# Kernel optimization log

Hardware: AMD Instinct MI355X
Metric: run time of the kernel (lower is better)

Reference implementation:

```python
import jax, jax.numpy as jnp
import numpy as np
import math

N_HEADS, INPUT_DIM, EMBED_DIM = 8, 512, 512
KEY_DIM = EMBED_DIM // N_HEADS  # val_dim == key_dim == 64
B, NQ, G = 4, 2048, 2048


def setup_inputs() -> dict:
    key = jax.random.key(0)
    ks = jax.random.split(key, 7)
    stdv_k = 1.0 / math.sqrt(KEY_DIM)
    stdv_e = 1.0 / math.sqrt(EMBED_DIM)
    return {
        "q": jax.random.normal(ks[0], (B, NQ, INPUT_DIM), jnp.float32),
        "h": jax.random.normal(ks[1], (B, G, INPUT_DIM), jnp.float32),
        "mask": jax.random.randint(ks[2], (B, NQ, G), 0, 2) == 1,  # True = attention not possible
        "W_query": jax.random.uniform(ks[3], (N_HEADS, INPUT_DIM, KEY_DIM), jnp.float32, -stdv_k, stdv_k),
        "W_key": jax.random.uniform(ks[4], (N_HEADS, INPUT_DIM, KEY_DIM), jnp.float32, -stdv_k, stdv_k),
        "W_val": jax.random.uniform(ks[5], (N_HEADS, INPUT_DIM, KEY_DIM), jnp.float32, -stdv_k, stdv_k),
        "W_out": jax.random.uniform(ks[6], (N_HEADS, KEY_DIM, EMBED_DIM), jnp.float32, -stdv_e, stdv_e),
    }


def reference(q, h, mask, W_query, W_key, W_val, W_out):
    norm = 1.0 / math.sqrt(KEY_DIM)
    # Per-head projections: (H, B, S, kd)
    Q = jnp.einsum("bqd,hdk->hbqk", q, W_query)
    K = jnp.einsum("bgd,hdk->hbgk", h, W_key)
    V = jnp.einsum("bgd,hdv->hbgv", h, W_val)
    # Full attention scores: (H, B, NQ, G)
    comp = norm * jnp.einsum("hbqk,hbgk->hbqg", Q, K)
    m = mask[None]  # (1, B, NQ, G) broadcasts over heads
    comp = jnp.where(m, -jnp.inf, comp)
    attn = jax.nn.softmax(comp, axis=-1)
    attn = jnp.where(m, 0.0, attn)  # mirrors the clone + zero step (also fixes all-masked rows)
    heads = jnp.einsum("hbqg,hbgv->hbqv", attn, V)
    # Output projection: flatten heads and apply W_out (H, vd, E)
    out = jnp.einsum("hbqv,hve->bqe", heads, W_out)
    return out
```

## Files before the change

### kernel.cpp

```cpp
#include <hip/hip_runtime.h>
#include <hip/hip_bf16.h>
#include <stdint.h>

#define NHEADS 8
#define INDIM 512
#define EMB 512
#define BSZ 4
#define NQS 2048
#define GS 2048

#define ALPHA_F 0.18033688011112042f

#if __has_builtin(__builtin_amdgcn_exp2f)
#define EXP2(x) __builtin_amdgcn_exp2f(x)
#else
#define EXP2(x) __expf((x)*0.69314718056f)
#endif

typedef short bf16x8 __attribute__((ext_vector_type(8)));
typedef float f32x4 __attribute__((ext_vector_type(4)));

static __device__ __forceinline__ unsigned short f2bf(float f) {
  unsigned int u = __builtin_bit_cast(unsigned int, f);
  unsigned int rounding = 0x7FFFu + ((u >> 16) & 1u);
  u += rounding;
  return (unsigned short)(u >> 16);
}

typedef __attribute__((address_space(3))) void lds_void;
typedef __attribute__((address_space(1))) const void gm_void;
static __device__ __forceinline__ void gll16(const void* g, void* s) {
  __builtin_amdgcn_global_load_lds((gm_void*)g, (lds_void*)s, 16, 0, 0);
}

__global__ void k_prep(const float4* __restrict__ q, const float4* __restrict__ h,
                       const void* __restrict__ mask,
                       const float* __restrict__ wq, const float* __restrict__ wk,
                       const float* __restrict__ wv, const float* __restrict__ wo,
                       ushort4* __restrict__ qb, ushort4* __restrict__ hb,
                       unsigned short* __restrict__ wqt, unsigned short* __restrict__ wkvt,
                       unsigned short* __restrict__ wot, unsigned short* __restrict__ maskB16) {
  int blk = blockIdx.x, t = threadIdx.x;
  if (blk < 2048) {
    const float4* src = blk < 1024 ? q : h;
    ushort4* dst = blk < 1024 ? qb : hb;
    int base = (blk & 1023) * 256 + t;
#pragma unroll
    for (int i = 0; i < 4; i++) {
      int idx = base + i * 262144;
      float4 v = src[idx];
      ushort4 o;
      o.x = f2bf(v.x); o.y = f2bf(v.y); o.z = f2bf(v.z); o.w = f2bf(v.w);
      dst[idx] = o;
    }
  } else if (blk < 3072) {
    const unsigned int* m32h = (const unsigned int*)mask;
    bool bytes = __ballot(m32h[t & 63] > 1u) != 0ull;
    int base = (blk - 2048) * 256 + t;
#pragma unroll
    for (int i = 0; i < 4; i++) {
      int widx = base + i * 262144;
      unsigned int bits = 0;
      if (bytes) {
        const uchar4* p = (const uchar4*)((const unsigned char*)mask + (size_t)widx * 16);
#pragma unroll
        for (int j = 0; j < 4; j++) {
          uchar4 v = p[j];
          bits |= ((v.x ? 1u : 0u) << (4 * j)) | ((v.y ? 1u : 0u) << (4 * j + 1)) |
                  ((v.z ? 1u : 0u) << (4 * j + 2)) | ((v.w ? 1u : 0u) << (4 * j + 3));
        }
      } else {
        const int4* p = (const int4*)((const int*)mask + (size_t)widx * 16);
#pragma unroll
        for (int j = 0; j < 4; j++) {
          int4 v = p[j];
          bits |= ((v.x ? 1u : 0u) << (4 * j)) | ((v.y ? 1u : 0u) << (4 * j + 1)) |
                  ((v.z ? 1u : 0u) << (4 * j + 2)) | ((v.w ? 1u : 0u) << (4 * j + 3));
        }
      }
      maskB16[widx] = (unsigned short)bits;
    }
  } else {
    int id = (blk - 3072) * 256 + t;
#pragma unroll
    for (int i = 0; i < 8; i++) {
      int e = id * 8 + i;
      int which = e >> 18, r = e & 262143;
      int k = r & 511, n = r >> 9;
      int hh = n >> 6, j = n & 63;
      if (which == 0) wqt[r] = f2bf(wq[hh * 32768 + k * 64 + j] * ALPHA_F);
      else if (which == 1) wkvt[r] = f2bf(wk[hh * 32768 + k * 64 + j]);
      else if (which == 2) wkvt[262144 + r] = f2bf(wv[hh * 32768 + k * 64 + j]);
      else wot[r] = f2bf(wo[k * 512 + n]);
    }
  }
}


template <int MODE>
__global__ __launch_bounds__(256) void k_gemm3(const unsigned short* __restrict__ A,
                                               const unsigned short* __restrict__ Bt,
                                               void* __restrict__ C, void* __restrict__ C2) {
  __shared__ unsigned short As[2][4096];
  __shared__ unsigned short Bs[2][8192];
  int m0 = blockIdx.x * 64, n0 = blockIdx.y * 128;
  int t = threadIdx.x;
  int w = t >> 6, l = t & 63, c = l & 15, lg = l >> 4;
  int wr = w >> 1, wc = w & 1;

  int rbA = t >> 7, kcc = (t >> 4) & 7, cc = t & 15;
  const unsigned short* aG = A + (size_t)(m0 + rbA * 16 + cc) * 512 + kcc * 8;
  const unsigned short* bG = Bt + (size_t)(n0 + rbA * 16 + cc) * 512 + kcc * 8;
  int ldsOff = w * 1024 + (t & 63) * 16;

  f32x4 acc[2][4];
#pragma unroll
  for (int mi = 0; mi < 2; mi++)
#pragma unroll
    for (int ni = 0; ni < 4; ni++) acc[mi][ni] = {0.f, 0.f, 0.f, 0.f};

  gll16(aG, (char*)As[0] + ldsOff);
  gll16(aG + 32 * 512, (char*)As[0] + ldsOff + 4096);
  gll16(bG, (char*)Bs[0] + ldsOff);
  gll16(bG + 32 * 512, (char*)Bs[0] + ldsOff + 4096);
  gll16(bG + 64 * 512, (char*)Bs[0] + ldsOff + 8192);
  gll16(bG + 96 * 512, (char*)Bs[0] + ldsOff + 12288);

  for (int kk = 0; kk < 8; kk++) {
    int cur = kk & 1;
    asm volatile("s_waitcnt vmcnt(0)" ::: "memory");
    __builtin_amdgcn_s_barrier();
    if (kk < 7) {
      int ko = (kk + 1) * 64;
      gll16(aG + ko, (char*)As[cur ^ 1] + ldsOff);
      gll16(aG + ko + 32 * 512, (char*)As[cur ^ 1] + ldsOff + 4096);
      gll16(bG + ko, (char*)Bs[cur ^ 1] + ldsOff);
      gll16(bG + ko + 32 * 512, (char*)Bs[cur ^ 1] + ldsOff + 4096);
      gll16(bG + ko + 64 * 512, (char*)Bs[cur ^ 1] + ldsOff + 8192);
      gll16(bG + ko + 96 * 512, (char*)Bs[cur ^ 1] + ldsOff + 12288);
    }
    bf16x8 af[2][2], bfr[4][2];
#pragma unroll
    for (int kc = 0; kc < 2; kc++) {
#pragma unroll
      for (int mi = 0; mi < 2; mi++)
        af[mi][kc] = *(const bf16x8*)((const char*)As[cur] + ((wr * 2 + mi) * 128 + (kc * 4 + lg) * 16 + c) * 16);
#pragma unroll
      for (int ni = 0; ni < 4; ni++)
        bfr[ni][kc] = *(const bf16x8*)((const char*)Bs[cur] + ((wc * 4 + ni) * 128 + (kc * 4 + lg) * 16 + c) * 16);
    }
#pragma unroll
    for (int kc = 0; kc < 2; kc++)
#pragma unroll
      for (int mi = 0; mi < 2; mi++)
#pragma unroll
        for (int ni = 0; ni < 4; ni++)
          acc[mi][ni] = __builtin_amdgcn_mfma_f32_16x16x32_bf16(af[mi][kc], bfr[ni][kc], acc[mi][ni], 0, 0, 0);
  }

#pragma unroll
  for (int mi = 0; mi < 2; mi++)
#pragma unroll
    for (int ni = 0; ni < 4; ni++) {
      int row = m0 + wr * 32 + mi * 16 + 4 * lg;
      int col = n0 + wc * 64 + ni * 16 + c;
#pragma unroll
      for (int r = 0; r < 4; r++)
        ((float*)C)[(size_t)(row + r) * 512 + col] = acc[mi][ni][r];
    }
}

__global__ __launch_bounds__(256) void k_gemmQKV(const unsigned short* __restrict__ qb_,
                                                 const unsigned short* __restrict__ hb_,
                                                 const unsigned short* __restrict__ wqt,
                                                 const unsigned short* __restrict__ wkvt,
                                                 unsigned short* __restrict__ Qp,
                                                 unsigned short* __restrict__ Kp,
                                                 unsigned short* __restrict__ Vt) {
  __shared__ unsigned short As[2][4096];
  __shared__ unsigned short Bs[2][8192];
  int ny = blockIdx.y;
  const unsigned short* A = (ny < 4) ? qb_ : hb_;
  const unsigned short* Bt = (ny < 4) ? wqt : wkvt;
  int n0 = (ny < 4) ? ny * 128 : (ny - 4) * 128;
  int m0 = blockIdx.x * 64;
  int t = threadIdx.x;
  int w = t >> 6, l = t & 63, c = l & 15, lg = l >> 4;
  int wr = w >> 1, wc = w & 1;

  int rbA = t >> 7, kcc = (t >> 4) & 7, cc = t & 15;
  const unsigned short* aG = A + (size_t)(m0 + rbA * 16 + cc) * 512 + kcc * 8;
  const unsigned short* bG = Bt + (size_t)(n0 + rbA * 16 + cc) * 512 + kcc * 8;
  int ldsOff = w * 1024 + (t & 63) * 16;

  f32x4 acc[2][4];
#pragma unroll
  for (int mi = 0; mi < 2; mi++)
#pragma unroll
    for (int ni = 0; ni < 4; ni++) acc[mi][ni] = {0.f, 0.f, 0.f, 0.f};

  gll16(aG, (char*)As[0] + ldsOff);
  gll16(aG + 32 * 512, (char*)As[0] + ldsOff + 4096);
  gll16(bG, (char*)Bs[0] + ldsOff);
  gll16(bG + 32 * 512, (char*)Bs[0] + ldsOff + 4096);
  gll16(bG + 64 * 512, (char*)Bs[0] + ldsOff + 8192);
  gll16(bG + 96 * 512, (char*)Bs[0] + ldsOff + 12288);

  for (int kk = 0; kk < 8; kk++) {
    int cur = kk & 1;
    asm volatile("s_waitcnt vmcnt(0)" ::: "memory");
    __builtin_amdgcn_s_barrier();
    if (kk < 7) {
      int ko = (kk + 1) * 64;
      gll16(aG + ko, (char*)As[cur ^ 1] + ldsOff);
      gll16(aG + ko + 32 * 512, (char*)As[cur ^ 1] + ldsOff + 4096);
      gll16(bG + ko, (char*)Bs[cur ^ 1] + ldsOff);
      gll16(bG + ko + 32 * 512, (char*)Bs[cur ^ 1] + ldsOff + 4096);
      gll16(bG + ko + 64 * 512, (char*)Bs[cur ^ 1] + ldsOff + 8192);
      gll16(bG + ko + 96 * 512, (char*)Bs[cur ^ 1] + ldsOff + 12288);
    }
    bf16x8 af[2][2], bfr[4][2];
#pragma unroll
    for (int kc = 0; kc < 2; kc++) {
#pragma unroll
      for (int mi = 0; mi < 2; mi++)
        af[mi][kc] = *(const bf16x8*)((const char*)As[cur] + ((wr * 2 + mi) * 128 + (kc * 4 + lg) * 16 + c) * 16);
#pragma unroll
      for (int ni = 0; ni < 4; ni++)
        bfr[ni][kc] = *(const bf16x8*)((const char*)Bs[cur] + ((wc * 4 + ni) * 128 + (kc * 4 + lg) * 16 + c) * 16);
    }
#pragma unroll
    for (int kc = 0; kc < 2; kc++)
#pragma unroll
      for (int mi = 0; mi < 2; mi++)
#pragma unroll
        for (int ni = 0; ni < 4; ni++)
          acc[mi][ni] = __builtin_amdgcn_mfma_f32_16x16x32_bf16(af[mi][kc], bfr[ni][kc], acc[mi][ni], 0, 0, 0);
  }

#pragma unroll
  for (int mi = 0; mi < 2; mi++)
#pragma unroll
    for (int ni = 0; ni < 4; ni++) {
      int row = m0 + wr * 32 + mi * 16 + 4 * lg;
      int col = n0 + wc * 64 + ni * 16 + c;
      if (ny < 4) {
#pragma unroll
        for (int r = 0; r < 4; r++)
          Qp[(size_t)(row + r) * 512 + col] = f2bf(acc[mi][ni][r]);
      } else if (col < 512) {
#pragma unroll
        for (int r = 0; r < 4; r++)
          Kp[(size_t)(row + r) * 512 + col] = f2bf(acc[mi][ni][r]);
      } else {
        int col5 = col - 512, hd2 = col5 >> 6, vv = col5 & 63;
        int bb = row >> 11, g = row & 2047;
        ushort4 u;
        u.x = f2bf(acc[mi][ni][0]);
        u.y = f2bf(acc[mi][ni][1]);
        u.z = f2bf(acc[mi][ni][2]);
        u.w = f2bf(acc[mi][ni][3]);
        *(ushort4*)(Vt + (size_t)((bb * 8 + hd2) * 64 + vv) * GS + g) = u;
      }
    }
}

__global__ __launch_bounds__(256) void k_attn6(const unsigned short* __restrict__ Qp,
                                               const unsigned short* __restrict__ Kp,
                                               const unsigned short* __restrict__ Vt,
                                               const unsigned short* __restrict__ maskB16,
                                               unsigned short* __restrict__ Hd) {
  __shared__ unsigned short Ksh[2][8192];
  __shared__ unsigned short Vsh[2][8192];
  __shared__ unsigned short Plds[4][2048];

  int bid = blockIdx.x;
  int fid = (bid & 7) * 64 + (bid >> 3);
  int qtile = fid & 15;
  int bh = fid >> 4;
  int b = bh >> 3, hd = bh & 7;

  int t = threadIdx.x;
  int w = t >> 6, l = t & 63, c = l & 15, lg = l >> 4;
  int qw = qtile * 128 + w * 32;

  bf16x8 qb[2][2];
#pragma unroll
  for (int qt = 0; qt < 2; qt++)
#pragma unroll
    for (int kc = 0; kc < 2; kc++)
      qb[qt][kc] = *(const bf16x8*)(Qp + (size_t)(b * NQS + qw + qt * 16 + c) * 512 + hd * 64 + kc * 32 + lg * 8);

  int sr = ((t >> 7) & 1) * 16 + (t & 15);
  int sdc = ((t >> 6) & 1) * 4 + ((t >> 4) & 3);
  const unsigned short* kgbase = Kp + (size_t)(b * GS + sr) * 512 + hd * 64 + sdc * 8;
  const unsigned short* vgbase = Vt + (size_t)(bh * 64 + sr) * GS + sdc * 8;
  char* kdst[2] = {(char*)&Ksh[0][0] + w * 1024, (char*)&Ksh[1][0] + w * 1024};
  char* vdst[2] = {(char*)&Vsh[0][0] + w * 1024, (char*)&Vsh[1][0] + w * 1024};

  f32x4 o[4][2];
#pragma unroll
  for (int vt = 0; vt < 4; vt++) { o[vt][0] = {0.f, 0.f, 0.f, 0.f}; o[vt][1] = {0.f, 0.f, 0.f, 0.f}; }
  float lrow[2] = {0.f, 0.f};

  const ulonglong2* mp0 = (const ulonglong2*)(maskB16 + (size_t)(b * NQS + qw + c) * 128);
  const ulonglong2* mp1 = (const ulonglong2*)(maskB16 + (size_t)(b * NQS + qw + 16 + c) * 128);

#pragma unroll
  for (int hh = 0; hh < 2; hh++) {
    const unsigned short* kg = kgbase + (size_t)(hh * 64) * 512;
    const unsigned short* vg = vgbase + hh * 64;
    gll16(kg, kdst[0] + hh * 8192);
    gll16(kg + 32 * 512, kdst[0] + hh * 8192 + 4096);
    gll16(vg, vdst[0] + hh * 8192);
    gll16(vg + 32 * GS, vdst[0] + hh * 8192 + 4096);
  }
  ulonglong2 m0 = mp0[0], m1 = mp1[0];
  ulonglong2 m0n = m0, m1n = m1;

  for (int kt = 0; kt < 16; kt++) {
    int cur = kt & 1;
    asm volatile("s_waitcnt vmcnt(0)" ::: "memory");
    __builtin_amdgcn_s_barrier();
    if (kt < 15) {
      size_t g0 = (size_t)(kt + 1) * 128;
#pragma unroll
      for (int hh = 0; hh < 2; hh++) {
        const unsigned short* kg = kgbase + (g0 + hh * 64) * 512;
        const unsigned short* vg = vgbase + g0 + hh * 64;
        char* kd = kdst[cur ^ 1] + hh * 8192;
        char* vd = vdst[cur ^ 1] + hh * 8192;
        gll16(kg, kd);
        gll16(kg + 32 * 512, kd + 4096);
        gll16(vg, vd);
        gll16(vg + 32 * GS, vd + 4096);
      }
      m0n = mp0[kt + 1];
      m1n = mp1[kt + 1];
    }

    f32x4 s0[4][2], s1[4][2];
#pragma unroll
    for (int gt = 0; gt < 4; gt++) {
      s0[gt][0] = {0.f, 0.f, 0.f, 0.f}; s0[gt][1] = {0.f, 0.f, 0.f, 0.f};
      s1[gt][0] = {0.f, 0.f, 0.f, 0.f}; s1[gt][1] = {0.f, 0.f, 0.f, 0.f};
    }
    const unsigned short* Kc0 = &Ksh[cur][0];
    const unsigned short* Kc1 = &Ksh[cur][4096];
    __builtin_amdgcn_s_setprio(1);
#pragma unroll
    for (int kc = 0; kc < 2; kc++) {
      bf16x8 ka[4];
#pragma unroll
      for (int gt = 0; gt < 4; gt++)
        ka[gt] = *(const bf16x8*)(Kc0 + ((gt * 2 + kc) * 64 + l) * 8);
#pragma unroll
      for (int gt = 0; gt < 4; gt++) {
        s0[gt][0] = __builtin_amdgcn_mfma_f32_16x16x32_bf16(ka[gt], qb[0][kc], s0[gt][0], 0, 0, 0);
        s0[gt][1] = __builtin_amdgcn_mfma_f32_16x16x32_bf16(ka[gt], qb[1][kc], s0[gt][1], 0, 0, 0);
      }
    }
#pragma unroll
    for (int kc = 0; kc < 2; kc++) {
      bf16x8 ka[4];
#pragma unroll
      for (int gt = 0; gt < 4; gt++)
        ka[gt] = *(const bf16x8*)(Kc1 + ((gt * 2 + kc) * 64 + l) * 8);
#pragma unroll
      for (int gt = 0; gt < 4; gt++) {
        s1[gt][0] = __builtin_amdgcn_mfma_f32_16x16x32_bf16(ka[gt], qb[0][kc], s1[gt][0], 0, 0, 0);
        s1[gt][1] = __builtin_amdgcn_mfma_f32_16x16x32_bf16(ka[gt], qb[1][kc], s1[gt][1], 0, 0, 0);
      }
    }
    __builtin_amdgcn_s_setprio(0);

#pragma unroll
    for (int qt = 0; qt < 2; qt++) {
      unsigned long long wmq = qt ? m1.x : m0.x;
      float ls = 0.f;
#pragma unroll
      for (int gt = 0; gt < 4; gt++) {
        unsigned nib = (unsigned)(wmq >> (gt * 16));
        f32x4 pv;
#pragma unroll
        for (int r = 0; r < 4; r++) {
          float e = EXP2(s0[gt][qt][r]);
          pv[r] = ((nib >> (4 * lg + r)) & 1u) ? 0.f : e;
          ls += pv[r];
        }
        s0[gt][qt] = pv;
      }
      lrow[qt] += ls;
#pragma unroll
      for (int gt = 0; gt < 4; gt++) {
        uint2 wp;
        asm("v_cvt_pk_bf16_f32 %0, %1, %2" : "=v"(wp.x) : "v"(s0[gt][qt][0]), "v"(s0[gt][qt][1]));
        asm("v_cvt_pk_bf16_f32 %0, %1, %2" : "=v"(wp.y) : "v"(s0[gt][qt][2]), "v"(s0[gt][qt][3]));
        int chunk = (qt * 2 + (gt >> 1)) * 64 + ((gt & 1) * 2 + (lg >> 1)) * 16 + c;
        *(uint2*)((char*)&Plds[w][0] + chunk * 16 + 8 * (lg & 1)) = wp;
      }
    }

#pragma unroll
    for (int qt = 0; qt < 2; qt++) {
      unsigned long long wmq = qt ? m1.y : m0.y;
      float ls = 0.f;
#pragma unroll
      for (int gt = 0; gt < 4; gt++) {
        unsigned nib = (unsigned)(wmq >> (gt * 16));
        f32x4 pv;
#pragma unroll
        for (int r = 0; r < 4; r++) {
          float e = EXP2(s1[gt][qt][r]);
          pv[r] = ((nib >> (4 * lg + r)) & 1u) ? 0.f : e;
          ls += pv[r];
        }
        s1[gt][qt] = pv;
      }
      lrow[qt] += ls;
    }

    asm volatile("s_waitcnt lgkmcnt(0)" ::: "memory");
    __builtin_amdgcn_sched_barrier(0);

    {
      const unsigned short* Vc = &Vsh[cur][0];
      __builtin_amdgcn_s_setprio(1);
#pragma unroll
      for (int kc2 = 0; kc2 < 2; kc2++) {
        bf16x8 pb[2];
#pragma unroll
        for (int qt = 0; qt < 2; qt++)
          pb[qt] = *(const bf16x8*)((const char*)&Plds[w][0] + ((qt * 2 + kc2) * 64 + l) * 16);
        bf16x8 va[4];
#pragma unroll
        for (int vt = 0; vt < 4; vt++)
          va[vt] = *(const bf16x8*)(Vc + ((vt * 2 + kc2) * 64 + l) * 8);
#pragma unroll
        for (int vt = 0; vt < 4; vt++) {
          o[vt][0] = __builtin_amdgcn_mfma_f32_16x16x32_bf16(va[vt], pb[0], o[vt][0], 0, 0, 0);
          o[vt][1] = __builtin_amdgcn_mfma_f32_16x16x32_bf16(va[vt], pb[1], o[vt][1], 0, 0, 0);
        }
      }
      __builtin_amdgcn_s_setprio(0);
    }
    __builtin_amdgcn_sched_barrier(0);

#pragma unroll
    for (int qt = 0; qt < 2; qt++)
#pragma unroll
      for (int gt = 0; gt < 4; gt++) {
        uint2 wp;
        asm("v_cvt_pk_bf16_f32 %0, %1, %2" : "=v"(wp.x) : "v"(s1[gt][qt][0]), "v"(s1[gt][qt][1]));
        asm("v_cvt_pk_bf16_f32 %0, %1, %2" : "=v"(wp.y) : "v"(s1[gt][qt][2]), "v"(s1[gt][qt][3]));
        int chunk = (qt * 2 + (gt >> 1)) * 64 + ((gt & 1) * 2 + (lg >> 1)) * 16 + c;
        *(uint2*)((char*)&Plds[w][0] + chunk * 16 + 8 * (lg & 1)) = wp;
      }
    asm volatile("s_waitcnt lgkmcnt(0)" ::: "memory");
    __builtin_amdgcn_sched_barrier(0);

    {
      const unsigned short* Vc = &Vsh[cur][4096];
      __builtin_amdgcn_s_setprio(1);
#pragma unroll
      for (int kc2 = 0; kc2 < 2; kc2++) {
        bf16x8 pb[2];
#pragma unroll
        for (int qt = 0; qt < 2; qt++)
          pb[qt] = *(const bf16x8*)((const char*)&Plds[w][0] + ((qt * 2 + kc2) * 64 + l) * 16);
        bf16x8 va[4];
#pragma unroll
        for (int vt = 0; vt < 4; vt++)
          va[vt] = *(const bf16x8*)(Vc + ((vt * 2 + kc2) * 64 + l) * 8);
#pragma unroll
        for (int vt = 0; vt < 4; vt++) {
          o[vt][0] = __builtin_amdgcn_mfma_f32_16x16x32_bf16(va[vt], pb[0], o[vt][0], 0, 0, 0);
          o[vt][1] = __builtin_amdgcn_mfma_f32_16x16x32_bf16(va[vt], pb[1], o[vt][1], 0, 0, 0);
        }
      }
      __builtin_amdgcn_s_setprio(0);
    }
    m0 = m0n;
    m1 = m1n;
  }

#pragma unroll
  for (int qt = 0; qt < 2; qt++) {
    float lr = lrow[qt];
    lr += __shfl_xor(lr, 16);
    lr += __shfl_xor(lr, 32);
    float inv = lr > 0.f ? 1.0f / lr : 0.f;
    int q = qw + qt * 16 + c;
#pragma unroll
    for (int vt = 0; vt < 4; vt++) {
      ushort4 u;
      u.x = f2bf(o[vt][qt][0] * inv);
      u.y = f2bf(o[vt][qt][1] * inv);
      u.z = f2bf(o[vt][qt][2] * inv);
      u.w = f2bf(o[vt][qt][3] * inv);
      *(ushort4*)(Hd + (size_t)(b * NQS + q) * 512 + hd * 64 + vt * 16 + 4 * lg) = u;
    }
  }
}


extern "C" void kernel_launch(void* const* d_in, const int* in_sizes, int n_in,
                              void* d_out, int out_size, void* d_ws, size_t ws_size,
                              hipStream_t stream) {
  const float* q = (const float*)d_in[0];
  const float* h = (const float*)d_in[1];
  const void* mask = d_in[2];
  const float* wq = (const float*)d_in[3];
  const float* wk = (const float*)d_in[4];
  const float* wv = (const float*)d_in[5];
  const float* wo = (const float*)d_in[6];
  float* out = (float*)d_out;

  unsigned short* qb_ = (unsigned short*)d_ws;
  unsigned short* hb_ = qb_ + 8192 * 512;
  unsigned short* Qp = hb_ + 8192 * 512;
  unsigned short* Kp = Qp + 8192 * 512;
  unsigned short* Vtp = Kp + 8192 * 512;
  unsigned short* Hd = Vtp + 8192 * 512;
  unsigned short* wqt = Hd + 8192 * 512;
  unsigned short* wkvt = wqt + 512 * 512;
  unsigned short* wot = wkvt + 1024 * 512;
  unsigned short* maskB16 = wot + 512 * 512;

  k_prep<<<3584, 256, 0, stream>>>((const float4*)q, (const float4*)h, mask, wq, wk, wv, wo,
                                   (ushort4*)qb_, (ushort4*)hb_, wqt, wkvt, wot, maskB16);
  dim3 gqkv(128, 12);
  k_gemmQKV<<<gqkv, 256, 0, stream>>>(qb_, hb_, wqt, wkvt, Qp, Kp, Vtp);
  k_attn6<<<512, 256, 0, stream>>>(Qp, Kp, Vtp, maskB16, Hd);
  dim3 go(128, 4);
  k_gemm3<1><<<go, 256, 0, stream>>>(Hd, wot, out, nullptr);
}
```

Baseline: 145.3 us.

## Rewrite attention with 32x32 MFMA, register-resident P, direct global K/V loads

Replaces the LDS double-buffered attention kernel with one that uses 32x32x16 MFMA tiles. K and V are read directly from global memory into registers, so there is no shared-memory staging and no block barriers. The probability matrix is repacked in registers with v_permlane32_swap instead of a round-trip through LDS. This removes LDS traffic and synchronization, but relies on cache hits for repeated K/V reads across waves and loses explicit prefetch overlap.

```diff
diff --git a/kernel.cpp b/kernel.cpp
--- a/kernel.cpp
+++ b/kernel.cpp
@@ -19,6 +19,8 @@
 
 typedef short bf16x8 __attribute__((ext_vector_type(8)));
 typedef float f32x4 __attribute__((ext_vector_type(4)));
+typedef float f32x16 __attribute__((ext_vector_type(16)));
+typedef unsigned int u32x4 __attribute__((ext_vector_type(4)));
 
 static __device__ __forceinline__ unsigned short f2bf(float f) {
   unsigned int u = __builtin_bit_cast(unsigned int, f);
@@ -95,7 +97,6 @@
     }
   }
 }
-
 
 template <int MODE>
 __global__ __launch_bounds__(256) void k_gemm3(const unsigned short* __restrict__ A,
@@ -265,15 +266,11 @@
     }
 }
 
-__global__ __launch_bounds__(256) void k_attn6(const unsigned short* __restrict__ Qp,
-                                               const unsigned short* __restrict__ Kp,
-                                               const unsigned short* __restrict__ Vt,
-                                               const unsigned short* __restrict__ maskB16,
-                                               unsigned short* __restrict__ Hd) {
-  __shared__ unsigned short Ksh[2][8192];
-  __shared__ unsigned short Vsh[2][8192];
-  __shared__ unsigned short Plds[4][2048];
-
+__global__ __launch_bounds__(256, 2) void k_attn7(const unsigned short* __restrict__ Qp,
+                                                  const unsigned short* __restrict__ Kp,
+                                                  const unsigned short* __restrict__ Vt,
+                                                  const unsigned short* __restrict__ maskB16,
+                                                  unsigned short* __restrict__ Hd) {
   int bid = blockIdx.x;
   int fid = (bid & 7) * 64 + (bid >> 3);
   int qtile = fid & 15;
@@ -281,224 +278,92 @@
   int b = bh >> 3, hd = bh & 7;
 
   int t = threadIdx.x;
-  int w = t >> 6, l = t & 63, c = l & 15, lg = l >> 4;
-  int qw = qtile * 128 + w * 32;
-
-  bf16x8 qb[2][2];
-#pragma unroll
-  for (int qt = 0; qt < 2; qt++)
-#pragma unroll
-    for (int kc = 0; kc < 2; kc++)
-      qb[qt][kc] = *(const bf16x8*)(Qp + (size_t)(b * NQS + qw + qt * 16 + c) * 512 + hd * 64 + kc * 32 + lg * 8);
-
-  int sr = ((t >> 7) & 1) * 16 + (t & 15);
-  int sdc = ((t >> 6) & 1) * 4 + ((t >> 4) & 3);
-  const unsigned short* kgbase = Kp + (size_t)(b * GS + sr) * 512 + hd * 64 + sdc * 8;
-  const unsigned short* vgbase = Vt + (size_t)(bh * 64 + sr) * GS + sdc * 8;
-  char* kdst[2] = {(char*)&Ksh[0][0] + w * 1024, (char*)&Ksh[1][0] + w * 1024};
-  char* vdst[2] = {(char*)&Vsh[0][0] + w * 1024, (char*)&Vsh[1][0] + w * 1024};
-
-  f32x4 o[4][2];
-#pragma unroll
-  for (int vt = 0; vt < 4; vt++) { o[vt][0] = {0.f, 0.f, 0.f, 0.f}; o[vt][1] = {0.f, 0.f, 0.f, 0.f}; }
-  float lrow[2] = {0.f, 0.f};
-
-  const ulonglong2* mp0 = (const ulonglong2*)(maskB16 + (size_t)(b * NQS + qw + c) * 128);
-  const ulonglong2* mp1 = (const ulonglong2*)(maskB16 + (size_t)(b * NQS + qw + 16 + c) * 128);
-
-#pragma unroll
-  for (int hh = 0; hh < 2; hh++) {
-    const unsigned short* kg = kgbase + (size_t)(hh * 64) * 512;
-    const unsigned short* vg = vgbase + hh * 64;
-    gll16(kg, kdst[0] + hh * 8192);
-    gll16(kg + 32 * 512, kdst[0] + hh * 8192 + 4096);
-    gll16(vg, vdst[0] + hh * 8192);
-    gll16(vg + 32 * GS, vdst[0] + hh * 8192 + 4096);
+  int w = t >> 6, l = t & 63;
+  int lo = l & 31, hi = l >> 5;
+  int hi4 = hi * 4;
+  int q = qtile * 128 + w * 32 + lo;
+
+  const unsigned short* qrow = Qp + (size_t)(b * NQS + q) * 512 + hd * 64 + hi * 8;
+  bf16x8 qf[4];
+#pragma unroll
+  for (int s = 0; s < 4; s++) qf[s] = *(const bf16x8*)(qrow + s * 16);
+
+  const unsigned short* krow = Kp + (size_t)(b * GS + lo) * 512 + hd * 64 + hi * 8;
+  const unsigned short* vrow0 = Vt + (size_t)(bh * 64 + lo) * GS + hi * 8;
+  const unsigned short* vrow1 = Vt + (size_t)(bh * 64 + 32 + lo) * GS + hi * 8;
+  const unsigned long long* mrow = (const unsigned long long*)maskB16 + (size_t)(b * NQS + q) * 32;
+
+  f32x16 o0, o1;
+#pragma unroll
+  for (int i = 0; i < 16; i++) { o0[i] = 0.f; o1[i] = 0.f; }
+  float ls[4] = {0.f, 0.f, 0.f, 0.f};
+
+  for (int kt = 0; kt < 32; kt++) {
+    unsigned long long wm = mrow[kt];
+#pragma unroll
+    for (int g2 = 0; g2 < 2; g2++) {
+      int gbase = kt * 64 + g2 * 32;
+      f32x16 sreg;
+#pragma unroll
+      for (int i = 0; i < 16; i++) sreg[i] = 0.f;
+#pragma unroll
+      for (int s = 0; s < 4; s++) {
+        bf16x8 ka = *(const bf16x8*)(krow + (size_t)gbase * 512 + s * 16);
+        sreg = __builtin_amdgcn_mfma_f32_32x32x16_bf16(ka, qf[s], sreg, 0, 0, 0);
+      }
+      unsigned int mbits = (unsigned int)(wm >> (g2 * 32));
+      float p[16];
+#pragma unroll
+      for (int r = 0; r < 16; r++) {
+        float e = EXP2(sreg[r]);
+        unsigned bit = (mbits >> ((r & 3) + 8 * (r >> 2) + hi4)) & 1u;
+        p[r] = bit ? 0.f : e;
+        ls[r & 3] += p[r];
+      }
+      unsigned int cw0, cw1, cw2, cw3, cw4, cw5, cw6, cw7;
+      asm("v_cvt_pk_bf16_f32 %0, %1, %2" : "=v"(cw0) : "v"(p[0]), "v"(p[1]));
+      asm("v_cvt_pk_bf16_f32 %0, %1, %2" : "=v"(cw1) : "v"(p[2]), "v"(p[3]));
+      asm("v_cvt_pk_bf16_f32 %0, %1, %2" : "=v"(cw2) : "v"(p[4]), "v"(p[5]));
+      asm("v_cvt_pk_bf16_f32 %0, %1, %2" : "=v"(cw3) : "v"(p[6]), "v"(p[7]));
+      asm("v_cvt_pk_bf16_f32 %0, %1, %2" : "=v"(cw4) : "v"(p[8]), "v"(p[9]));
+      asm("v_cvt_pk_bf16_f32 %0, %1, %2" : "=v"(cw5) : "v"(p[10]), "v"(p[11]));
+      asm("v_cvt_pk_bf16_f32 %0, %1, %2" : "=v"(cw6) : "v"(p[12]), "v"(p[13]));
+      asm("v_cvt_pk_bf16_f32 %0, %1, %2" : "=v"(cw7) : "v"(p[14]), "v"(p[15]));
+      asm("v_permlane32_swap_b32 %0, %1" : "+v"(cw0), "+v"(cw2));
+      asm("v_permlane32_swap_b32 %0, %1" : "+v"(cw1), "+v"(cw3));
+      asm("v_permlane32_swap_b32 %0, %1" : "+v"(cw4), "+v"(cw6));
+      asm("v_permlane32_swap_b32 %0, %1" : "+v"(cw5), "+v"(cw7));
+      u32x4 pw0 = {cw0, cw1, cw2, cw3};
+      u32x4 pw1 = {cw4, cw5, cw6, cw7};
+      bf16x8 pb0 = __builtin_bit_cast(bf16x8, pw0);
+      bf16x8 pb1 = __builtin_bit_cast(bf16x8, pw1);
+      bf16x8 va00 = *(const bf16x8*)(vrow0 + gbase);
+      bf16x8 va10 = *(const bf16x8*)(vrow1 + gbase);
+      bf16x8 va01 = *(const bf16x8*)(vrow0 + gbase + 16);
+      bf16x8 va11 = *(const bf16x8*)(vrow1 + gbase + 16);
+      o0 = __builtin_amdgcn_mfma_f32_32x32x16_bf16(va00, pb0, o0, 0, 0, 0);
+      o1 = __builtin_amdgcn_mfma_f32_32x32x16_bf16(va10, pb0, o1, 0, 0, 0);
+      o0 = __builtin_amdgcn_mfma_f32_32x32x16_bf16(va01, pb1, o0, 0, 0, 0);
+      o1 = __builtin_amdgcn_mfma_f32_32x32x16_bf16(va11, pb1, o1, 0, 0, 0);
+    }
   }
-  ulonglong2 m0 = mp0[0], m1 = mp1[0];
-  ulonglong2 m0n = m0, m1n = m1;
-
-  for (int kt = 0; kt < 16; kt++) {
-    int cur = kt & 1;
-    asm volatile("s_waitcnt vmcnt(0)" ::: "memory");
-    __builtin_amdgcn_s_barrier();
-    if (kt < 15) {
-      size_t g0 = (size_t)(kt + 1) * 128;
-#pragma unroll
-      for (int hh = 0; hh < 2; hh++) {
-        const unsigned short* kg = kgbase + (g0 + hh * 64) * 512;
-        const unsigned short* vg = vgbase + g0 + hh * 64;
-        char* kd = kdst[cur ^ 1] + hh * 8192;
-        char* vd = vdst[cur ^ 1] + hh * 8192;
-        gll16(kg, kd);
-        gll16(kg + 32 * 512, kd + 4096);
-        gll16(vg, vd);
-        gll16(vg + 32 * GS, vd + 4096);
-      }
-      m0n = mp0[kt + 1];
-      m1n = mp1[kt + 1];
-    }
-
-    f32x4 s0[4][2], s1[4][2];
-#pragma unroll
-    for (int gt = 0; gt < 4; gt++) {
-      s0[gt][0] = {0.f, 0.f, 0.f, 0.f}; s0[gt][1] = {0.f, 0.f, 0.f, 0.f};
-      s1[gt][0] = {0.f, 0.f, 0.f, 0.f}; s1[gt][1] = {0.f, 0.f, 0.f, 0.f};
-    }
-    const unsigned short* Kc0 = &Ksh[cur][0];
-    const unsigned short* Kc1 = &Ksh[cur][4096];
-    __builtin_amdgcn_s_setprio(1);
-#pragma unroll
-    for (int kc = 0; kc < 2; kc++) {
-      bf16x8 ka[4];
-#pragma unroll
-      for (int gt = 0; gt < 4; gt++)
-        ka[gt] = *(const bf16x8*)(Kc0 + ((gt * 2 + kc) * 64 + l) * 8);
-#pragma unroll
-      for (int gt = 0; gt < 4; gt++) {
-        s0[gt][0] = __builtin_amdgcn_mfma_f32_16x16x32_bf16(ka[gt], qb[0][kc], s0[gt][0], 0, 0, 0);
-        s0[gt][1] = __builtin_amdgcn_mfma_f32_16x16x32_bf16(ka[gt], qb[1][kc], s0[gt][1], 0, 0, 0);
-      }
-    }
-#pragma unroll
-    for (int kc = 0; kc < 2; kc++) {
-      bf16x8 ka[4];
-#pragma unroll
-      for (int gt = 0; gt < 4; gt++)
-        ka[gt] = *(const bf16x8*)(Kc1 + ((gt * 2 + kc) * 64 + l) * 8);
-#pragma unroll
-      for (int gt = 0; gt < 4; gt++) {
-        s1[gt][0] = __builtin_amdgcn_mfma_f32_16x16x32_bf16(ka[gt], qb[0][kc], s1[gt][0], 0, 0, 0);
-        s1[gt][1] = __builtin_amdgcn_mfma_f32_16x16x32_bf16(ka[gt], qb[1][kc], s1[gt][1], 0, 0, 0);
-      }
-    }
-    __builtin_amdgcn_s_setprio(0);
-
-#pragma unroll
-    for (int qt = 0; qt < 2; qt++) {
-      unsigned long long wmq = qt ? m1.x : m0.x;
-      float ls = 0.f;
-#pragma unroll
-      for (int gt = 0; gt < 4; gt++) {
-        unsigned nib = (unsigned)(wmq >> (gt * 16));
-        f32x4 pv;
-#pragma unroll
-        for (int r = 0; r < 4; r++) {
-          float e = EXP2(s0[gt][qt][r]);
-          pv[r] = ((nib >> (4 * lg + r)) & 1u) ? 0.f : e;
-          ls += pv[r];
-        }
-        s0[gt][qt] = pv;
-      }
-      lrow[qt] += ls;
-#pragma unroll
-      for (int gt = 0; gt < 4; gt++) {
-        uint2 wp;
-        asm("v_cvt_pk_bf16_f32 %0, %1, %2" : "=v"(wp.x) : "v"(s0[gt][qt][0]), "v"(s0[gt][qt][1]));
-        asm("v_cvt_pk_bf16_f32 %0, %1, %2" : "=v"(wp.y) : "v"(s0[gt][qt][2]), "v"(s0[gt][qt][3]));
-        int chunk = (qt * 2 + (gt >> 1)) * 64 + ((gt & 1) * 2 + (lg >> 1)) * 16 + c;
-        *(uint2*)((char*)&Plds[w][0] + chunk * 16 + 8 * (lg & 1)) = wp;
-      }
-    }
-
-#pragma unroll
-    for (int qt = 0; qt < 2; qt++) {
-      unsigned long long wmq = qt ? m1.y : m0.y;
-      float ls = 0.f;
-#pragma unroll
-      for (int gt = 0; gt < 4; gt++) {
-        unsigned nib = (unsigned)(wmq >> (gt * 16));
-        f32x4 pv;
-#pragma unroll
-        for (int r = 0; r < 4; r++) {
-          float e = EXP2(s1[gt][qt][r]);
-          pv[r] = ((nib >> (4 * lg + r)) & 1u) ? 0.f : e;
-          ls += pv[r];
-        }
-        s1[gt][qt] = pv;
-      }
-      lrow[qt] += ls;
-    }
-
-    asm volatile("s_waitcnt lgkmcnt(0)" ::: "memory");
-    __builtin_amdgcn_sched_barrier(0);
-
-    {
-      const unsigned short* Vc = &Vsh[cur][0];
-      __builtin_amdgcn_s_setprio(1);
-#pragma unroll
-      for (int kc2 = 0; kc2 < 2; kc2++) {
-        bf16x8 pb[2];
-#pragma unroll
-        for (int qt = 0; qt < 2; qt++)
-          pb[qt] = *(const bf16x8*)((const char*)&Plds[w][0] + ((qt * 2 + kc2) * 64 + l) * 16);
-        bf16x8 va[4];
-#pragma unroll
-        for (int vt = 0; vt < 4; vt++)
-          va[vt] = *(const bf16x8*)(Vc + ((vt * 2 + kc2) * 64 + l) * 8);
-#pragma unroll
-        for (int vt = 0; vt < 4; vt++) {
-          o[vt][0] = __builtin_amdgcn_mfma_f32_16x16x32_bf16(va[vt], pb[0], o[vt][0], 0, 0, 0);
-          o[vt][1] = __builtin_amdgcn_mfma_f32_16x16x32_bf16(va[vt], pb[1], o[vt][1], 0, 0, 0);
-        }
-      }
-      __builtin_amdgcn_s_setprio(0);
-    }
-    __builtin_amdgcn_sched_barrier(0);
-
-#pragma unroll
-    for (int qt = 0; qt < 2; qt++)
-#pragma unroll
-      for (int gt = 0; gt < 4; gt++) {
-        uint2 wp;
-        asm("v_cvt_pk_bf16_f32 %0, %1, %2" : "=v"(wp.x) : "v"(s1[gt][qt][0]), "v"(s1[gt][qt][1]));
-        asm("v_cvt_pk_bf16_f32 %0, %1, %2" : "=v"(wp.y) : "v"(s1[gt][qt][2]), "v"(s1[gt][qt][3]));
-        int chunk = (qt * 2 + (gt >> 1)) * 64 + ((gt & 1) * 2 + (lg >> 1)) * 16 + c;
-        *(uint2*)((char*)&Plds[w][0] + chunk * 16 + 8 * (lg & 1)) = wp;
-      }
-    asm volatile("s_waitcnt lgkmcnt(0)" ::: "memory");
-    __builtin_amdgcn_sched_barrier(0);
-
-    {
-      const unsigned short* Vc = &Vsh[cur][4096];
-      __builtin_amdgcn_s_setprio(1);
-#pragma unroll
-      for (int kc2 = 0; kc2 < 2; kc2++) {
-        bf16x8 pb[2];
-#pragma unroll
-        for (int qt = 0; qt < 2; qt++)
-          pb[qt] = *(const bf16x8*)((const char*)&Plds[w][0] + ((qt * 2 + kc2) * 64 + l) * 16);
-        bf16x8 va[4];
-#pragma unroll
-        for (int vt = 0; vt < 4; vt++)
-          va[vt] = *(const bf16x8*)(Vc + ((vt * 2 + kc2) * 64 + l) * 8);
-#pragma unroll
-        for (int vt = 0; vt < 4; vt++) {
-          o[vt][0] = __builtin_amdgcn_mfma_f32_16x16x32_bf16(va[vt], pb[0], o[vt][0], 0, 0, 0);
-          o[vt][1] = __builtin_amdgcn_mfma_f32_16x16x32_bf16(va[vt], pb[1], o[vt][1], 0, 0, 0);
-        }
-      }
-      __builtin_amdgcn_s_setprio(0);
-    }
-    m0 = m0n;
-    m1 = m1n;
-  }
-
-#pragma unroll
-  for (int qt = 0; qt < 2; qt++) {
-    float lr = lrow[qt];
-    lr += __shfl_xor(lr, 16);
-    lr += __shfl_xor(lr, 32);
-    float inv = lr > 0.f ? 1.0f / lr : 0.f;
-    int q = qw + qt * 16 + c;
-#pragma unroll
-    for (int vt = 0; vt < 4; vt++) {
+
+  float lsum = (ls[0] + ls[1]) + (ls[2] + ls[3]);
+  lsum += __shfl_xor(lsum, 32);
+  float inv = lsum > 0.f ? 1.0f / lsum : 0.f;
+  unsigned short* hrow = Hd + (size_t)(b * NQS + q) * 512 + hd * 64;
+#pragma unroll
+  for (int vt = 0; vt < 2; vt++) {
+#pragma unroll
+    for (int gr = 0; gr < 4; gr++) {
       ushort4 u;
-      u.x = f2bf(o[vt][qt][0] * inv);
-      u.y = f2bf(o[vt][qt][1] * inv);
-      u.z = f2bf(o[vt][qt][2] * inv);
-      u.w = f2bf(o[vt][qt][3] * inv);
-      *(ushort4*)(Hd + (size_t)(b * NQS + q) * 512 + hd * 64 + vt * 16 + 4 * lg) = u;
+      float v0 = (vt ? o1[gr * 4 + 0] : o0[gr * 4 + 0]) * inv;
+      float v1 = (vt ? o1[gr * 4 + 1] : o0[gr * 4 + 1]) * inv;
+      float v2 = (vt ? o1[gr * 4 + 2] : o0[gr * 4 + 2]) * inv;
+      float v3 = (vt ? o1[gr * 4 + 3] : o0[gr * 4 + 3]) * inv;
+      u.x = f2bf(v0); u.y = f2bf(v1); u.z = f2bf(v2); u.w = f2bf(v3);
+      int vv = vt * 32 + 8 * gr + hi4;
+      *(ushort4*)(hrow + vv) = u;
     }
   }
 }
@@ -531,7 +396,7 @@
                                    (ushort4*)qb_, (ushort4*)hb_, wqt, wkvt, wot, maskB16);
   dim3 gqkv(128, 12);
   k_gemmQKV<<<gqkv, 256, 0, stream>>>(qb_, hb_, wqt, wkvt, Qp, Kp, Vtp);
-  k_attn6<<<512, 256, 0, stream>>>(Qp, Kp, Vtp, maskB16, Hd);
+  k_attn7<<<512, 256, 0, stream>>>(Qp, Kp, Vtp, maskB16, Hd);
   dim3 go(128, 4);
   k_gemm3<1><<<go, 256, 0, stream>>>(Hd, wot, out, nullptr);
 }
```

Result: slower. 218.8 us (+50.5%).
